# Performance work log

Measured on AMD Instinct MI355X. Metric: run time of the kernel, lower is better.

The kernel has to match this reference:

```python
import jax, jax.numpy as jnp
import numpy as np

HEADS = 16
DIM_HEAD = 64
SCALE = DIM_HEAD ** -0.5


def shift(x):
    # Transformer-XL relative shift trick. x: [..., i, j] -> [..., i, j]
    *pre, i, j = x.shape
    x = jnp.concatenate([x, jnp.zeros((*pre, i, i), x.dtype)], axis=-1)
    l = i + j - 1
    x = x.reshape(*pre, -1)
    pad = (-x.shape[-1]) % l
    x = jnp.concatenate([x, jnp.zeros((*pre, pad), x.dtype)], axis=-1)
    x = x.reshape(*pre, -1, l)
    return x[..., :i, i - 1:]


def setup_inputs() -> dict:
    key = jax.random.key(0)
    ks = jax.random.split(key, 8)
    b, t, e = 2, 1024, 1024
    mem_len, lmem_len = 1024, 128
    kv_len = t + mem_len + lmem_len
    return {
        "x": jax.random.normal(ks[0], (b, t, e), jnp.float32),
        "mem": jax.random.normal(ks[1], (b, mem_len, e), jnp.float32),
        "lmem": jax.random.normal(ks[2], (b, lmem_len, e), jnp.float32),
        "pos_emb": jax.random.normal(ks[3], (HEADS, kv_len, DIM_HEAD), jnp.float32),
        "input_mask": jnp.ones((b, t), bool),
        "Wq": jax.random.normal(ks[4], (e, e), jnp.float32) * 0.02,
        "Wkv": jax.random.normal(ks[5], (e, 2 * e), jnp.float32) * 0.02,
        "Wout": jax.random.normal(ks[6], (e, e), jnp.float32) * 0.02,
        "bout": jnp.zeros((e,), jnp.float32),
    }


def reference(x, mem, lmem, pos_emb, input_mask, Wq, Wkv, Wout, bout):
    b, t, e = x.shape
    h, dh = HEADS, DIM_HEAD
    mem_len, lmem_len = mem.shape[1], lmem.shape[1]
    total_mem = mem_len + lmem_len

    q = x @ Wq
    kv_input = jnp.concatenate([lmem, mem, x], axis=1)  # [b, kv_len, e]
    kv_len = kv_input.shape[1]
    k, v = jnp.split(kv_input @ Wkv, 2, axis=-1)

    def merge_heads(z):
        return z.reshape(b, -1, h, dh).transpose(0, 2, 1, 3)  # [b, h, n, dh]

    q, k, v = merge_heads(q), merge_heads(k), merge_heads(v)

    dots = jnp.einsum('bhid,bhjd->bhij', q, k) * SCALE  # [b, h, t, kv_len]

    pe = pos_emb[:, -kv_len:].astype(q.dtype)
    pos_dots = jnp.einsum('bhid,hjd->bhij', q, pe) * SCALE
    dots = dots + shift(pos_dots)

    mask_value = -jnp.finfo(dots.dtype).max

    pad_mask = input_mask[:, None, :, None] & input_mask[:, None, None, :]
    pad_mask = jnp.pad(pad_mask, ((0, 0), (0, 0), (0, 0), (total_mem, 0)), constant_values=True)
    dots = jnp.where(pad_mask, dots, mask_value)

    causal = jnp.triu(jnp.ones((t, t + total_mem), bool), k=1 + total_mem)
    dots = jnp.where(causal[None, None], mask_value, dots)

    attn = jax.nn.softmax(dots, axis=-1)
    out = jnp.einsum('bhij,bhjd->bhid', attn, v)
    out = out.transpose(0, 2, 1, 3).reshape(b, t, -1)
    return out @ Wout + bout
```

## Files before the change

### kernel.cpp

```cpp
#include <hip/hip_runtime.h>


typedef unsigned int   u32;
typedef unsigned short u16;
typedef unsigned long long u64;
typedef __attribute__((ext_vector_type(8))) short short8;
typedef __attribute__((ext_vector_type(4))) float f32x4;
typedef __attribute__((ext_vector_type(4))) u32   u32x4;

#define DEVI static __device__ __forceinline__
#define MFMA_BF16 __builtin_amdgcn_mfma_f32_16x16x32_bf16

DEVI u16 f2bf(float f) {
  u32 u = __builtin_bit_cast(u32, f);
  return (u16)((u + 0x7FFFu + ((u >> 16) & 1u)) >> 16);
}
DEVI float bf2f(u16 h) { u32 u = (u32)h << 16; return __builtin_bit_cast(float, u); }
DEVI u32 pk2(float lo, float hi) { return (u32)f2bf(lo) | ((u32)f2bf(hi) << 16); }

constexpr int T_ = 1024, E_ = 1024, KV = 2176, H_ = 16;

__global__ void k_prep_kvin(const float* __restrict__ x, const float* __restrict__ mem,
                            const float* __restrict__ lmem, u16* __restrict__ kvin) {
  int u = blockIdx.x * 256 + threadIdx.x;
  int b = u / (KV * E_ / 8);
  int r = u % (KV * E_ / 8);
  int j = r >> 7;
  int e8 = (r & 127) << 3;
  const float* src;
  if (j < 128)        src = lmem + ((size_t)(b * 128 + j) * E_ + e8);
  else if (j < 1152)  src = mem  + ((size_t)(b * 1024 + (j - 128)) * E_ + e8);
  else                src = x    + ((size_t)(b * 1024 + (j - 1152)) * E_ + e8);
  float4 a = ((const float4*)src)[0];
  float4 c = ((const float4*)src)[1];
  u32x4 o = { pk2(a.x, a.y), pk2(a.z, a.w), pk2(c.x, c.y), pk2(c.z, c.w) };
  *(u32x4*)(kvin + (size_t)u * 8) = o;
}

__global__ void k_prep_pe(const float* __restrict__ pos, u16* __restrict__ pe) {
  size_t u = (size_t)blockIdx.x * 256 + threadIdx.x;
  float4 a = ((const float4*)(pos + u * 8))[0];
  float4 c = ((const float4*)(pos + u * 8))[1];
  u32x4 o = { pk2(a.x, a.y), pk2(a.z, a.w), pk2(c.x, c.y), pk2(c.z, c.w) };
  *(u32x4*)(pe + u * 8) = o;
}

__global__ void k_transp(const float* __restrict__ src, u16* __restrict__ dst, int K, int N) {
  __shared__ float tile[32][33];
  int n0 = blockIdx.x * 32, k0 = blockIdx.y * 32;
  int tx = threadIdx.x, ty = threadIdx.y;
#pragma unroll
  for (int s = 0; s < 4; s++) tile[ty + 8 * s][tx] = src[(size_t)(k0 + ty + 8 * s) * N + n0 + tx];
  __syncthreads();
#pragma unroll
  for (int s = 0; s < 4; s++)
    dst[(size_t)(n0 + ty + 8 * s) * K + k0 + tx] = f2bf(tile[tx][ty + 8 * s]);
}

__global__ __launch_bounds__(256, 2)
void k_gemm_qkv(const u16* __restrict__ kvin, const u16* __restrict__ WallT,
                u16* __restrict__ qb, u16* __restrict__ kb, u16* __restrict__ vtb) {
  int bid = blockIdx.x;
  int b = bid / 336;
  int r = bid % 336;
  int nt, mt;
  if (r < 64) { nt = r >> 3; mt = 9 + (r & 7); }
  else { r -= 64; nt = 8 + r / 17; mt = r % 17; }

  const u16* A  = kvin + ((size_t)b * KV + (size_t)mt * 128) * E_;
  const u16* Bm = WallT + (size_t)nt * 128 * E_;

  __shared__ u16 As[128 * 40];
  __shared__ u16 Bs[128 * 40];

  int t = threadIdx.x;
  int wid = t >> 6, lane = t & 63;
  int wr = wid >> 1, wc = wid & 1;
  int l15 = lane & 15, l4 = lane >> 4;

  f32x4 acc[4][4] = {};
  int arow = t >> 2, aslot = t & 3;

  u32x4 ra[2], rb[2];
#pragma unroll
  for (int p = 0; p < 2; p++) {
    ra[p] = *(const u32x4*)(A  + (size_t)(arow + 64 * p) * E_ + aslot * 8);
    rb[p] = *(const u32x4*)(Bm + (size_t)(arow + 64 * p) * E_ + aslot * 8);
  }
  for (int kt = 0; kt < 32; kt++) {
    __syncthreads();
#pragma unroll
    for (int p = 0; p < 2; p++) {
      *(u32x4*)(As + (arow + 64 * p) * 40 + aslot * 8) = ra[p];
      *(u32x4*)(Bs + (arow + 64 * p) * 40 + aslot * 8) = rb[p];
    }
    __syncthreads();
    if (kt + 1 < 32) {
      int k0 = (kt + 1) * 32;
#pragma unroll
      for (int p = 0; p < 2; p++) {
        ra[p] = *(const u32x4*)(A  + (size_t)(arow + 64 * p) * E_ + k0 + aslot * 8);
        rb[p] = *(const u32x4*)(Bm + (size_t)(arow + 64 * p) * E_ + k0 + aslot * 8);
      }
    }
    short8 af[4], bfv[4];
#pragma unroll
    for (int m = 0; m < 4; m++)
      af[m] = *(const short8*)(As + (wr * 64 + m * 16 + l15) * 40 + l4 * 8);
#pragma unroll
    for (int n = 0; n < 4; n++)
      bfv[n] = *(const short8*)(Bs + (wc * 64 + n * 16 + l15) * 40 + l4 * 8);
#pragma unroll
    for (int m = 0; m < 4; m++)
#pragma unroll
      for (int n = 0; n < 4; n++)
        acc[m][n] = MFMA_BF16(af[m], bfv[n], acc[m][n], 0, 0, 0);
  }
  int grow_base = mt * 128 + wr * 64;
  int ncol_base = nt * 128 + wc * 64;
  if (nt < 8) {
#pragma unroll
    for (int m = 0; m < 4; m++)
#pragma unroll
      for (int n = 0; n < 4; n++) {
        int col = ncol_base + n * 16 + l15;
        int head = col >> 6, d = col & 63;
#pragma unroll
        for (int rg = 0; rg < 4; rg++) {
          int row = grow_base + m * 16 + l4 * 4 + rg - 1152;
          qb[(((size_t)b * 16 + head) * 1024 + row) * 64 + d] = f2bf(acc[m][n][rg] * 0.125f);
        }
      }
  } else if (nt < 16) {
#pragma unroll
    for (int m = 0; m < 4; m++)
#pragma unroll
      for (int n = 0; n < 4; n++) {
        int c = ncol_base + n * 16 + l15 - 1024;
        int head = c >> 6, d = c & 63;
#pragma unroll
        for (int rg = 0; rg < 4; rg++) {
          int row = grow_base + m * 16 + l4 * 4 + rg;
          kb[(((size_t)b * 16 + head) * KV + row) * 64 + d] = f2bf(acc[m][n][rg]);
        }
      }
  } else {
#pragma unroll
    for (int m = 0; m < 4; m++)
#pragma unroll
      for (int n = 0; n < 4; n++) {
        int c = ncol_base + n * 16 + l15 - 2048;
        int head = c >> 6, d = c & 63;
        int jb = grow_base + m * 16 + l4 * 4;
        u64 pv = (u64)f2bf(acc[m][n][0]) | ((u64)f2bf(acc[m][n][1]) << 16)
               | ((u64)f2bf(acc[m][n][2]) << 32) | ((u64)f2bf(acc[m][n][3]) << 48);
        *(u64*)(vtb + (((size_t)b * 16 + head) * 64 + d) * KV + jb) = pv;
      }
  }
}

__global__ __launch_bounds__(256, 2)
void k_attn(const u16* __restrict__ qb, const u16* __restrict__ kb,
            const u16* __restrict__ vtb, const u16* __restrict__ peb,
            u16* __restrict__ ao) {
  int bid = blockIdx.x;
  int xcd = bid & 7, bk = bid >> 3;
  int it = bk & 15, g = bk >> 4;
  int bh = g * 8 + xcd;
  int b = bh >> 4, h = bh & 15;
  int i0 = it * 64;

  __shared__ u16 Klds[2][64][72];
  __shared__ u16 Vt[2][64][72];
  __shared__ u16 Band[64][136];
  __shared__ u16 Pb[4][16][72];

  int t = threadIdx.x, wid = t >> 6, lane = t & 63;
  int l15 = lane & 15, l4 = lane >> 4;
  int il = wid * 16 + l15;
  int srow = t >> 3, ssl = t & 7;

  const u16* kbase  = kb  + (size_t)bh * KV * 64;
  const u16* vtbase = vtb + (size_t)bh * 64 * KV;
  const u16* pebase = peb + (size_t)h * KV * 64;

  const u16* qptr = qb + ((size_t)bh * 1024 + i0 + il) * 64 + l4 * 8;
  short8 qf0 = *(const short8*)qptr;
  short8 qf1 = *(const short8*)(qptr + 32);

  f32x4 Of[4] = {};
  float mr = -1e30f, lr = 0.f;
  int njt = it + 19;

  u32x4 rk0, rk1, rv0, rv1;
  auto load_regs = [&](int jt_) {
    int j0_ = jt_ * 64;
    rk0 = *(const u32x4*)(kbase + (size_t)(j0_ + srow) * 64 + ssl * 8);
    rk1 = *(const u32x4*)(kbase + (size_t)(j0_ + srow + 32) * 64 + ssl * 8);
    rv0 = *(const u32x4*)(vtbase + (size_t)srow * KV + j0_ + ssl * 8);
    rv1 = *(const u32x4*)(vtbase + (size_t)(srow + 32) * KV + j0_ + ssl * 8);
  };
  auto store_tile = [&](int buf) {
    *(u32x4*)(&Klds[buf][srow][ssl * 8]) = rk0;
    *(u32x4*)(&Klds[buf][srow + 32][ssl * 8]) = rk1;
    *(u32x4*)(&Vt[buf][srow][ssl * 8]) = rv0;
    *(u32x4*)(&Vt[buf][srow + 32][ssl * 8]) = rv1;
  };
  auto load_pe = [&](int prb, short8* pf) {
#pragma unroll
    for (int rc = 0; rc < 4; rc++) {
      int rr = prb + rc * 16 + l15; rr = rr > 2175 ? 2175 : rr;
#pragma unroll
      for (int kk = 0; kk < 2; kk++)
        pf[rc * 2 + kk] = *(const short8*)(pebase + (size_t)rr * 64 + kk * 32 + l4 * 8);
    }
  };
  auto band_mfma_store = [&](int prb, const short8* pf) {
    __builtin_amdgcn_s_setprio(1);
    f32x4 acc[4];
#pragma unroll
    for (int rc = 0; rc < 4; rc++) {
      f32x4 a = {};
      a = MFMA_BF16(pf[rc * 2 + 0], qf0, a, 0, 0, 0);
      a = MFMA_BF16(pf[rc * 2 + 1], qf1, a, 0, 0, 0);
      acc[rc] = a;
    }
    __builtin_amdgcn_s_setprio(0);
#pragma unroll
    for (int rc = 0; rc < 4; rc++) {
      int rb = prb + rc * 16 + l4 * 4 + il + 1;
#pragma unroll
      for (int rg = 0; rg < 4; rg++)
        Band[il][(rb + rg) & 127] = f2bf(acc[rc][rg]);
    }
  };

  load_regs(0);
  store_tile(0);
  {
    short8 pf[8];
    load_pe(960 - i0, pf);
    band_mfma_store(960 - i0, pf);
  }
  load_regs(1);

  int cur = 0;
  for (int jt = 0; jt < njt; jt++) {
    bool domask = (jt == njt - 1);
    __syncthreads();

    short8 pf[8];
    load_pe(1024 + 64 * jt - i0, pf);

    f32x4 sc[4];
    __builtin_amdgcn_s_setprio(1);
#pragma unroll
    for (int jc = 0; jc < 4; jc++) {
      f32x4 a = {};
      short8 k0 = *(const short8*)(&Klds[cur][jc * 16 + l15][l4 * 8]);
      short8 k1 = *(const short8*)(&Klds[cur][jc * 16 + l15][32 + l4 * 8]);
      a = MFMA_BF16(k0, qf0, a, 0, 0, 0);
      a = MFMA_BF16(k1, qf1, a, 0, 0, 0);
      sc[jc] = a;
    }
    __builtin_amdgcn_s_setprio(0);

    band_mfma_store(1024 + 64 * jt - i0, pf);

    short8 vf[8];
#pragma unroll
    for (int df = 0; df < 4; df++)
#pragma unroll
      for (int kk = 0; kk < 2; kk++)
        vf[df * 2 + kk] = *(const short8*)(&Vt[cur][df * 16 + l15][kk * 32 + l4 * 8]);

    asm volatile("s_waitcnt lgkmcnt(0)" ::: "memory");
    __builtin_amdgcn_sched_barrier(0);

    float P[4][4];
    float mx = -1e30f;
    int cb0 = ((jt - it) & 1) << 6;
#pragma unroll
    for (int jc = 0; jc < 4; jc++) {
      u64 bl = *(const u64*)(&Band[il][cb0 + jc * 16 + l4 * 4]);
#pragma unroll
      for (int rg = 0; rg < 4; rg++) {
        int jj = jc * 16 + l4 * 4 + rg;
        float v = sc[jc][rg] + bf2f((u16)(bl >> (16 * rg)));
        if (domask && (jj > il)) v = -1e30f;
        P[jc][rg] = v;
        mx = fmaxf(mx, v);
      }
    }
    mx = fmaxf(mx, __shfl_xor(mx, 16, 64));
    mx = fmaxf(mx, __shfl_xor(mx, 32, 64));
    float mnew = fmaxf(mr, mx);
    float fac = __expf(mr - mnew);
    mr = mnew;
    float ps = 0.f;
#pragma unroll
    for (int jc = 0; jc < 4; jc++)
#pragma unroll
      for (int rg = 0; rg < 4; rg++) {
        float p = __expf(P[jc][rg] - mnew);
        P[jc][rg] = p;
        ps += p;
      }
    ps += __shfl_xor(ps, 16, 64);
    ps += __shfl_xor(ps, 32, 64);
    lr = lr * fac + ps;
#pragma unroll
    for (int dc = 0; dc < 4; dc++) Of[dc] *= fac;

#pragma unroll
    for (int jc = 0; jc < 4; jc++)
#pragma unroll
      for (int rg = 0; rg < 4; rg++)
        Pb[wid][l15][jc * 16 + l4 * 4 + rg] = f2bf(P[jc][rg]);

    asm volatile("s_waitcnt lgkmcnt(0)" ::: "memory");
    __builtin_amdgcn_sched_barrier(0);

    short8 pB0 = *(const short8*)(&Pb[wid][l15][l4 * 8]);
    short8 pB1 = *(const short8*)(&Pb[wid][l15][32 + l4 * 8]);
    __builtin_amdgcn_s_setprio(1);
#pragma unroll
    for (int df = 0; df < 4; df++) {
      Of[df] = MFMA_BF16(vf[df * 2 + 0], pB0, Of[df], 0, 0, 0);
      Of[df] = MFMA_BF16(vf[df * 2 + 1], pB1, Of[df], 0, 0, 0);
    }
    __builtin_amdgcn_s_setprio(0);

    if (jt + 1 < njt) {
      store_tile(cur ^ 1);
      if (jt + 2 < njt) load_regs(jt + 2);
    }
    cur ^= 1;
  }

  float inv = 1.0f / lr;
  size_t ob = ((size_t)b * 1024 + i0 + il) * 1024 + h * 64;
#pragma unroll
  for (int df = 0; df < 4; df++) {
    u64 pv = (u64)f2bf(Of[df][0] * inv)         | ((u64)f2bf(Of[df][1] * inv) << 16)
           | ((u64)f2bf(Of[df][2] * inv) << 32) | ((u64)f2bf(Of[df][3] * inv) << 48);
    *(u64*)(ao + ob + df * 16 + l4 * 4) = pv;
  }
}

__global__ __launch_bounds__(256, 2)
void k_gemm_out(const u16* __restrict__ ao, const u16* __restrict__ WoT,
                const float* __restrict__ bias, float* __restrict__ out) {
  int mt = blockIdx.x & 31, nt = blockIdx.x >> 5;
  const u16* A  = ao  + (size_t)mt * 64 * E_;
  const u16* Bm = WoT + (size_t)nt * 128 * E_;
  __shared__ u16 As[64 * 40];
  __shared__ u16 Bs[128 * 40];
  int t = threadIdx.x, wid = t >> 6, lane = t & 63;
  int wr = wid >> 1, wc = wid & 1, l15 = lane & 15, l4 = lane >> 4;
  f32x4 acc[2][4] = {};
  int arow = t >> 2, aslot = t & 3;

  u32x4 ra, rb[2];
  ra = *(const u32x4*)(A + (size_t)arow * E_ + aslot * 8);
#pragma unroll
  for (int p = 0; p < 2; p++)
    rb[p] = *(const u32x4*)(Bm + (size_t)(arow + 64 * p) * E_ + aslot * 8);
  for (int kt = 0; kt < 32; kt++) {
    __syncthreads();
    *(u32x4*)(As + arow * 40 + aslot * 8) = ra;
#pragma unroll
    for (int p = 0; p < 2; p++)
      *(u32x4*)(Bs + (arow + 64 * p) * 40 + aslot * 8) = rb[p];
    __syncthreads();
    if (kt + 1 < 32) {
      int k0 = (kt + 1) * 32;
      ra = *(const u32x4*)(A + (size_t)arow * E_ + k0 + aslot * 8);
#pragma unroll
      for (int p = 0; p < 2; p++)
        rb[p] = *(const u32x4*)(Bm + (size_t)(arow + 64 * p) * E_ + k0 + aslot * 8);
    }
    short8 af[2], bfv[4];
#pragma unroll
    for (int m = 0; m < 2; m++)
      af[m] = *(const short8*)(As + (wr * 32 + m * 16 + l15) * 40 + l4 * 8);
#pragma unroll
    for (int n = 0; n < 4; n++)
      bfv[n] = *(const short8*)(Bs + (wc * 64 + n * 16 + l15) * 40 + l4 * 8);
#pragma unroll
    for (int m = 0; m < 2; m++)
#pragma unroll
      for (int n = 0; n < 4; n++)
        acc[m][n] = MFMA_BF16(af[m], bfv[n], acc[m][n], 0, 0, 0);
  }
#pragma unroll
  for (int n = 0; n < 4; n++) {
    int col = nt * 128 + wc * 64 + n * 16 + l15;
    float bv = bias[col];
#pragma unroll
    for (int m = 0; m < 2; m++) {
      int row = mt * 64 + wr * 32 + m * 16 + l4 * 4;
#pragma unroll
      for (int rg = 0; rg < 4; rg++)
        out[(size_t)(row + rg) * E_ + col] = acc[m][n][rg] + bv;
    }
  }
}

extern "C" void kernel_launch(void* const* d_in, const int* in_sizes, int n_in,
                              void* d_out, int out_size, void* d_ws, size_t ws_size,
                              hipStream_t stream) {
  (void)in_sizes; (void)n_in; (void)out_size; (void)ws_size;
  const float* x    = (const float*)d_in[0];
  const float* mem  = (const float*)d_in[1];
  const float* lmem = (const float*)d_in[2];
  const float* pos  = (const float*)d_in[3];
  const float* Wq   = (const float*)d_in[5];
  const float* Wkv  = (const float*)d_in[6];
  const float* Wout = (const float*)d_in[7];
  const float* bout = (const float*)d_in[8];
  float* out = (float*)d_out;

  u16* kvin  = (u16*)d_ws;
  u16* pe    = kvin  + (size_t)2 * KV * E_;
  u16* WallT = pe    + (size_t)H_ * KV * 64;
  u16* WoT   = WallT + (size_t)3072 * E_;
  u16* qb    = WoT   + (size_t)E_ * E_;
  u16* kb    = qb    + (size_t)2 * H_ * T_ * 64;
  u16* vtb   = kb    + (size_t)2 * H_ * KV * 64;
  u16* ao    = vtb   + (size_t)2 * H_ * KV * 64;

  k_prep_kvin<<<2176, 256, 0, stream>>>(x, mem, lmem, kvin);
  k_prep_pe<<<1088, 256, 0, stream>>>(pos, pe);
  k_transp<<<dim3(32, 32), dim3(32, 8), 0, stream>>>(Wq,   WallT,             1024, 1024);
  k_transp<<<dim3(64, 32), dim3(32, 8), 0, stream>>>(Wkv,  WallT + 1024*1024, 1024, 2048);
  k_transp<<<dim3(32, 32), dim3(32, 8), 0, stream>>>(Wout, WoT,               1024, 1024);
  k_gemm_qkv<<<672, 256, 0, stream>>>(kvin, WallT, qb, kb, vtb);
  k_attn<<<512, 256, 0, stream>>>(qb, kb, vtb, pe, ao);
  k_gemm_out<<<256, 256, 0, stream>>>(ao, WoT, bout, out);
}
```

Measured before the change: 160.1 us.

## Double-buffer QKV GEMM, prefetch PE, lazy softmax rescale, exp2 and packed bf16 converts

The QKV GEMM now uses double-buffered shared tiles, which drops one barrier per k-step and overlaps the global loads with MFMA work. In attention, positional-embedding fragments are prefetched one tile ahead, and Q is pre-scaled by log2(e) so softmax can use exp2. The running-max rescale is skipped unless the max grows by more than 8, and bf16 packing uses the hardware v_cvt_pk_bf16_f32 instruction. Block-to-tile mapping is reversed for half of the head groups to balance causal work. The costs are more LDS and register pressure, and a small numerical risk from the lazy rescale threshold.

Result: faster. 146.6 us (-8.5%).

```diff
diff --git a/kernel.cpp b/kernel.cpp
--- a/kernel.cpp
+++ b/kernel.cpp
@@ -17,8 +17,14 @@
 }
 DEVI float bf2f(u16 h) { u32 u = (u32)h << 16; return __builtin_bit_cast(float, u); }
 DEVI u32 pk2(float lo, float hi) { return (u32)f2bf(lo) | ((u32)f2bf(hi) << 16); }
+DEVI u32 cvtpk(float lo, float hi) {
+  u32 r;
+  asm("v_cvt_pk_bf16_f32 %0, %1, %2" : "=v"(r) : "v"(lo), "v"(hi));
+  return r;
+}
 
 constexpr int T_ = 1024, E_ = 1024, KV = 2176, H_ = 16;
+constexpr float QSCALE = 0.125f * 1.44269504088896f;
 
 __global__ void k_prep_kvin(const float* __restrict__ x, const float* __restrict__ mem,
                             const float* __restrict__ lmem, u16* __restrict__ kvin) {
@@ -70,8 +76,8 @@
   const u16* A  = kvin + ((size_t)b * KV + (size_t)mt * 128) * E_;
   const u16* Bm = WallT + (size_t)nt * 128 * E_;
 
-  __shared__ u16 As[128 * 40];
-  __shared__ u16 Bs[128 * 40];
+  __shared__ u16 As[2][128 * 40];
+  __shared__ u16 Bs[2][128 * 40];
 
   int t = threadIdx.x;
   int wid = t >> 6, lane = t & 63;
@@ -82,39 +88,40 @@
   int arow = t >> 2, aslot = t & 3;
 
   u32x4 ra[2], rb[2];
-#pragma unroll
-  for (int p = 0; p < 2; p++) {
-    ra[p] = *(const u32x4*)(A  + (size_t)(arow + 64 * p) * E_ + aslot * 8);
-    rb[p] = *(const u32x4*)(Bm + (size_t)(arow + 64 * p) * E_ + aslot * 8);
-  }
+  auto ld = [&](int kt_) {
+    int k0 = kt_ * 32;
+#pragma unroll
+    for (int p = 0; p < 2; p++) {
+      ra[p] = *(const u32x4*)(A  + (size_t)(arow + 64 * p) * E_ + k0 + aslot * 8);
+      rb[p] = *(const u32x4*)(Bm + (size_t)(arow + 64 * p) * E_ + k0 + aslot * 8);
+    }
+  };
+  auto st = [&](int buf) {
+#pragma unroll
+    for (int p = 0; p < 2; p++) {
+      *(u32x4*)(As[buf] + (arow + 64 * p) * 40 + aslot * 8) = ra[p];
+      *(u32x4*)(Bs[buf] + (arow + 64 * p) * 40 + aslot * 8) = rb[p];
+    }
+  };
+
+  ld(0); st(0); ld(1);
   for (int kt = 0; kt < 32; kt++) {
     __syncthreads();
-#pragma unroll
-    for (int p = 0; p < 2; p++) {
-      *(u32x4*)(As + (arow + 64 * p) * 40 + aslot * 8) = ra[p];
-      *(u32x4*)(Bs + (arow + 64 * p) * 40 + aslot * 8) = rb[p];
-    }
-    __syncthreads();
-    if (kt + 1 < 32) {
-      int k0 = (kt + 1) * 32;
-#pragma unroll
-      for (int p = 0; p < 2; p++) {
-        ra[p] = *(const u32x4*)(A  + (size_t)(arow + 64 * p) * E_ + k0 + aslot * 8);
-        rb[p] = *(const u32x4*)(Bm + (size_t)(arow + 64 * p) * E_ + k0 + aslot * 8);
-      }
-    }
+    int buf = kt & 1;
     short8 af[4], bfv[4];
 #pragma unroll
     for (int m = 0; m < 4; m++)
-      af[m] = *(const short8*)(As + (wr * 64 + m * 16 + l15) * 40 + l4 * 8);
+      af[m] = *(const short8*)(As[buf] + (wr * 64 + m * 16 + l15) * 40 + l4 * 8);
 #pragma unroll
     for (int n = 0; n < 4; n++)
-      bfv[n] = *(const short8*)(Bs + (wc * 64 + n * 16 + l15) * 40 + l4 * 8);
+      bfv[n] = *(const short8*)(Bs[buf] + (wc * 64 + n * 16 + l15) * 40 + l4 * 8);
 #pragma unroll
     for (int m = 0; m < 4; m++)
 #pragma unroll
       for (int n = 0; n < 4; n++)
         acc[m][n] = MFMA_BF16(af[m], bfv[n], acc[m][n], 0, 0, 0);
+    if (kt + 1 < 32) st(buf ^ 1);
+    if (kt + 2 < 32) ld(kt + 2);
   }
   int grow_base = mt * 128 + wr * 64;
   int ncol_base = nt * 128 + wc * 64;
@@ -128,7 +135,7 @@
 #pragma unroll
         for (int rg = 0; rg < 4; rg++) {
           int row = grow_base + m * 16 + l4 * 4 + rg - 1152;
-          qb[(((size_t)b * 16 + head) * 1024 + row) * 64 + d] = f2bf(acc[m][n][rg] * 0.125f);
+          qb[(((size_t)b * 16 + head) * 1024 + row) * 64 + d] = f2bf(acc[m][n][rg] * QSCALE);
         }
       }
   } else if (nt < 16) {
@@ -164,8 +171,10 @@
             const u16* __restrict__ vtb, const u16* __restrict__ peb,
             u16* __restrict__ ao) {
   int bid = blockIdx.x;
-  int xcd = bid & 7, bk = bid >> 3;
-  int it = bk & 15, g = bk >> 4;
+  int xcd = bid & 7;
+  int itr = (bid >> 3) & 15;
+  int g   = bid >> 7;
+  int it  = (g >= 2) ? (15 - itr) : itr;
   int bh = g * 8 + xcd;
   int b = bh >> 4, h = bh & 15;
   int i0 = it * 64;
@@ -216,8 +225,8 @@
     }
   };
   auto band_mfma_store = [&](int prb, const short8* pf) {
+    f32x4 acc[4];
     __builtin_amdgcn_s_setprio(1);
-    f32x4 acc[4];
 #pragma unroll
     for (int rc = 0; rc < 4; rc++) {
       f32x4 a = {};
@@ -229,28 +238,27 @@
 #pragma unroll
     for (int rc = 0; rc < 4; rc++) {
       int rb = prb + rc * 16 + l4 * 4 + il + 1;
-#pragma unroll
-      for (int rg = 0; rg < 4; rg++)
-        Band[il][(rb + rg) & 127] = f2bf(acc[rc][rg]);
+      u32 w01 = cvtpk(acc[rc][0], acc[rc][1]);
+      u32 w23 = cvtpk(acc[rc][2], acc[rc][3]);
+      Band[il][rb & 127]       = (u16)w01;
+      Band[il][(rb + 1) & 127] = (u16)(w01 >> 16);
+      Band[il][(rb + 2) & 127] = (u16)w23;
+      Band[il][(rb + 3) & 127] = (u16)(w23 >> 16);
     }
   };
 
   load_regs(0);
   store_tile(0);
-  {
-    short8 pf[8];
-    load_pe(960 - i0, pf);
-    band_mfma_store(960 - i0, pf);
-  }
+  short8 pf[8];
+  load_pe(960 - i0, pf);
+  band_mfma_store(960 - i0, pf);
+  load_pe(1024 - i0, pf);
   load_regs(1);
 
   int cur = 0;
   for (int jt = 0; jt < njt; jt++) {
     bool domask = (jt == njt - 1);
     __syncthreads();
-
-    short8 pf[8];
-    load_pe(1024 + 64 * jt - i0, pf);
 
     f32x4 sc[4];
     __builtin_amdgcn_s_setprio(1);
@@ -266,6 +274,7 @@
     __builtin_amdgcn_s_setprio(0);
 
     band_mfma_store(1024 + 64 * jt - i0, pf);
+    if (jt + 1 < njt) load_pe(1024 + 64 * (jt + 1) - i0, pf);
 
     short8 vf[8];
 #pragma unroll
@@ -294,30 +303,33 @@
     }
     mx = fmaxf(mx, __shfl_xor(mx, 16, 64));
     mx = fmaxf(mx, __shfl_xor(mx, 32, 64));
-    float mnew = fmaxf(mr, mx);
-    float fac = __expf(mr - mnew);
-    mr = mnew;
+    if (!__all(mx <= mr + 8.0f)) {
+      float mnew = fmaxf(mr, mx);
+      float fac = exp2f(mr - mnew);
+      mr = mnew;
+      lr *= fac;
+#pragma unroll
+      for (int dc = 0; dc < 4; dc++) Of[dc] *= fac;
+    }
     float ps = 0.f;
 #pragma unroll
     for (int jc = 0; jc < 4; jc++)
 #pragma unroll
       for (int rg = 0; rg < 4; rg++) {
-        float p = __expf(P[jc][rg] - mnew);
+        float p = exp2f(P[jc][rg] - mr);
         P[jc][rg] = p;
         ps += p;
       }
     ps += __shfl_xor(ps, 16, 64);
     ps += __shfl_xor(ps, 32, 64);
-    lr = lr * fac + ps;
-#pragma unroll
-    for (int dc = 0; dc < 4; dc++) Of[dc] *= fac;
-
-#pragma unroll
-    for (int jc = 0; jc < 4; jc++)
-#pragma unroll
-      for (int rg = 0; rg < 4; rg++)
-        Pb[wid][l15][jc * 16 + l4 * 4 + rg] = f2bf(P[jc][rg]);
-
+    lr += ps;
+
+#pragma unroll
+    for (int jc = 0; jc < 4; jc++) {
+      int cb = jc * 16 + l4 * 4;
+      *(u32*)(&Pb[wid][l15][cb])     = cvtpk(P[jc][0], P[jc][1]);
+      *(u32*)(&Pb[wid][l15][cb + 2]) = cvtpk(P[jc][2], P[jc][3]);
+    }
     asm volatile("s_waitcnt lgkmcnt(0)" ::: "memory");
     __builtin_amdgcn_sched_barrier(0);
 
```
